# Performance work log

Measured on AMD Instinct MI355X. Metric: run time of the kernel, lower is better.

Reference implementation:

```python
import jax, jax.numpy as jnp
import numpy as np

B, N, DIM, VDIM, H, HD = 4, 1369, 1024, 1536, 16, 64
ROPE_HW, ROPE_DIM, THETA = 37, 32, 10000.0
LN_EPS = 1e-5


def _rope_tables():
    # VisionRotaryEmbeddingFast: freqs_for='lang', dim=32, pt_seq_len=ft_seq_len=37
    inv = 1.0 / THETA ** (jnp.arange(0, ROPE_DIM, 2, dtype=jnp.float32) / ROPE_DIM)  # [16]
    t = jnp.arange(ROPE_HW, dtype=jnp.float32) / ROPE_HW * ROPE_HW                    # [37]
    f = t[:, None] * inv[None, :]                                                     # [37,16]
    f = jnp.repeat(f, 2, axis=-1)                                                     # [37,32]
    # broadcat along last dim over the 2D grid -> [37,37,64]
    f2 = jnp.concatenate([jnp.broadcast_to(f[:, None, :], (ROPE_HW, ROPE_HW, ROPE_DIM)),
                          jnp.broadcast_to(f[None, :, :], (ROPE_HW, ROPE_HW, ROPE_DIM))], axis=-1)
    f2 = f2.reshape(-1, 2 * ROPE_DIM)                                                 # [1369,64]
    return jnp.cos(f2), jnp.sin(f2)


def _rotate_half(x):
    # pairs (x0,x1) -> (-x1,x0), interleaved
    xr = x.reshape(*x.shape[:-1], x.shape[-1] // 2, 2)
    x1, x2 = xr[..., 0], xr[..., 1]
    return jnp.stack((-x2, x1), axis=-1).reshape(x.shape)


def setup_inputs() -> dict:
    key = jax.random.key(0)
    ks = jax.random.split(key, 8)
    return {
        "x": jax.random.normal(ks[0], (B, N, DIM), jnp.float32),
        "value": jax.random.normal(ks[1], (B, N, VDIM), jnp.float32),
        "attn_mask": jax.random.randint(ks[2], (B, N), 0, 2).astype(bool),
        "wq": jax.random.normal(ks[3], (DIM, DIM), jnp.float32) * 0.02,
        "wk": jax.random.normal(ks[4], (DIM, VDIM), jnp.float32) * 0.02,
        "wv": jax.random.normal(ks[5], (DIM, VDIM), jnp.float32) * 0.02,
        "ln_g": jnp.ones((DIM,), jnp.float32),
        "ln_b": jnp.zeros((DIM,), jnp.float32),
        "wp": jax.random.normal(ks[6], (DIM, DIM), jnp.float32) * 0.02,
        "bp": jnp.zeros((DIM,), jnp.float32),
    }


def reference(x, value, attn_mask, wq, wk, wv, ln_g, ln_b, wp, bp):
    cos, sin = _rope_tables()  # [N, 64] each
    # projections (torch F.linear: y = x @ W.T)
    q = jnp.einsum('bni,oi->bno', x, wq).reshape(B, N, H, HD).transpose(0, 2, 1, 3)
    k = jnp.einsum('bni,oi->bno', value, wk).reshape(B, N, H, HD).transpose(0, 2, 1, 3)
    v = jnp.einsum('bni,oi->bno', value, wv).reshape(B, N, H, HD).transpose(0, 2, 1, 3)
    # inline RoPE on q and k
    q = q * cos + _rotate_half(q) * sin
    k = k * cos + _rotate_half(k) * sin
    q = q * (HD ** -0.5)
    attn = jnp.einsum('bhnd,bhmd->bhnm', q, k)
    neg_inf = jnp.finfo(attn.dtype).min
    attn = jnp.where(attn_mask[:, None, None, :], attn, neg_inf)
    attn = jax.nn.softmax(attn, axis=-1)
    out = jnp.einsum('bhnm,bhmd->bhnd', attn, v)
    out = out.transpose(0, 2, 1, 3).reshape(B, N, H * HD)
    # inner_attn_ln (LayerNorm, eps=1e-5)
    mu = jnp.mean(out, axis=-1, keepdims=True)
    var = jnp.var(out, axis=-1, keepdims=True)
    out = (out - mu) * jax.lax.rsqrt(var + LN_EPS) * ln_g + ln_b
    # output projection
    return jnp.einsum('bni,oi->bno', out, wp) + bp
```

## Files before the change

kernel.cpp:

```cpp
#include <hip/hip_runtime.h>
#include <hip/hip_bf16.h>

#define BB 4
#define NN 1369
#define DIMM 1024
#define VDIMM 1536
#define HH 16
#define MM (BB*NN)
#define MPAD 5504
#define NPAD 1408
#define KVB 64
#define NT (NPAD/KVB)
#define QSCALE 0.18028334f

typedef __attribute__((ext_vector_type(4))) float f32x4;
typedef __attribute__((ext_vector_type(8))) __bf16 bf16x8;
typedef __attribute__((ext_vector_type(4))) __bf16 bf16x4;

#define GLOAD_LDS(gsrc, ldst) \
  __builtin_amdgcn_global_load_lds((const __attribute__((address_space(1))) unsigned int*)(gsrc), \
                                   (__attribute__((address_space(3))) unsigned int*)(ldst), 16, 0, 0)

__global__ __launch_bounds__(256) void cvt4(const float* __restrict__ src,
                                            __bf16* __restrict__ dst, int n4) {
  int i = blockIdx.x * blockDim.x + threadIdx.x;
  int st = gridDim.x * blockDim.x;
  for (; i < n4; i += st) {
    f32x4 v = ((const f32x4*)src)[i];
    bf16x4 o;
    o[0] = (__bf16)v[0]; o[1] = (__bf16)v[1];
    o[2] = (__bf16)v[2]; o[3] = (__bf16)v[3];
    ((bf16x4*)dst)[i] = o;
  }
}

__global__ __launch_bounds__(256) void rope_tables(float* __restrict__ cosT,
                                                   float* __restrict__ sinT) {
  int idx = blockIdx.x * blockDim.x + threadIdx.x;
  if (idx >= NN * 64) return;
  int n = idx >> 6, d = idx & 63;
  int r = n / 37, c = n % 37;
  int m = (d < 32) ? (d >> 1) : ((d - 32) >> 1);
  float p = (d < 32) ? (float)r : (float)c;
  float inv = powf(10000.f, -(float)m * (1.f / 16.f));
  float a = p * inv;
  cosT[idx] = cosf(a);
  sinT[idx] = sinf(a);
}

__global__ __launch_bounds__(256) void mask_prep(const void* __restrict__ mask,
                                                 float* __restrict__ maskA) {
  __shared__ int flags[2];
  int t = threadIdx.x;
  if (t < 2) flags[t] = 0;
  __syncthreads();
  const unsigned int* mw = (const unsigned int*)mask;
  for (int i = t; i < NN; i += blockDim.x) {
    unsigned int w = mw[i];
    if (w == 0x3F800000u) atomicOr(&flags[1], 1);
    else if (w > 1u) atomicOr(&flags[0], 1);
  }
  __syncthreads();
  int md = flags[1] ? 2 : (flags[0] ? 1 : 0);
  const unsigned char* mb = (const unsigned char*)mask;
  const float* mf = (const float*)mask;
  for (int i = t; i < BB * NPAD; i += blockDim.x) {
    int b = i / NPAD, key = i % NPAD;
    float v = -1e30f;
    if (key < NN) {
      int idx = b * NN + key;
      bool on = (md == 0) ? (mw[idx] != 0u) : (md == 1) ? (mb[idx] != 0) : (mf[idx] != 0.f);
      if (on) v = 0.f;
    }
    maskA[i] = v;
  }
}

template <int TN, int EPI>
__global__ __launch_bounds__(256) void gemm_bt(
    const __bf16* __restrict__ A, const __bf16* __restrict__ W, int K,
    __bf16* __restrict__ obf, __bf16* __restrict__ obf2, float* __restrict__ of32,
    const float* __restrict__ cosT, const float* __restrict__ sinT,
    const float* __restrict__ bp) {
  constexpr int MI = (TN == 128) ? 4 : 2;
  __shared__ __bf16 As[3][128 * 32];
  __shared__ __bf16 Bs[3][TN * 32];
  const int tid = threadIdx.x;
  const int w = tid >> 6, l = tid & 63;
  const int i0 = blockIdx.x;
  const int orig = (i0 & 7) * 86 + (i0 >> 3);
  const int tN = orig & 15, tM = orig >> 4;
  const int wm = (TN == 128) ? (w >> 1) : w;
  const int wn = (TN == 128) ? (w & 1) : 0;
  const int wmo = wm * ((TN == 128) ? 64 : 32);
  const int lo = l & 15, hi = l >> 4;

  const __bf16* Asrc = A + (size_t)(tM * 128 + lo) * K + hi * 8;
  const __bf16* Wsrc = W + (size_t)(tN * TN + lo) * K + hi * 8;

  f32x4 zero = {0.f, 0.f, 0.f, 0.f};
  f32x4 acc[MI][4];
#pragma unroll
  for (int i = 0; i < MI; ++i)
#pragma unroll
    for (int j = 0; j < 4; ++j) acc[i][j] = zero;

  auto GSTAGE = [&](int buf, int k0) {
#pragma unroll
    for (int j = 0; j < 2; ++j) {
      const int c = j * 4 + w;
      GLOAD_LDS(Asrc + (size_t)c * 16 * K + k0, (char*)&As[buf][c * 512]);
    }
    if constexpr (TN == 128) {
#pragma unroll
      for (int j = 0; j < 2; ++j) {
        const int c = j * 4 + w;
        GLOAD_LDS(Wsrc + (size_t)c * 16 * K + k0, (char*)&Bs[buf][c * 512]);
      }
    } else {
      GLOAD_LDS(Wsrc + (size_t)w * 16 * K + k0, (char*)&Bs[buf][w * 512]);
    }
  };

  const int nk = K >> 5;
  GSTAGE(0, 0);
  GSTAGE(1, 32);
  const int ga = wmo >> 4;
  const int gb = (TN == 128) ? (wn * 4) : 0;
  for (int t = 0; t < nk; ++t) {
    if (t < nk - 1) {
      if constexpr (TN == 128) asm volatile("s_waitcnt vmcnt(4)" ::: "memory");
      else                     asm volatile("s_waitcnt vmcnt(3)" ::: "memory");
    } else {
      asm volatile("s_waitcnt vmcnt(0)" ::: "memory");
    }
    asm volatile("s_barrier" ::: "memory");
    const int cb = t % 3;
    bf16x8 af[MI], bfr[4];
#pragma unroll
    for (int mi = 0; mi < MI; ++mi)
      af[mi] = *(const bf16x8*)&As[cb][(ga + mi) * 512 + hi * 128 + lo * 8];
#pragma unroll
    for (int ni = 0; ni < 4; ++ni)
      bfr[ni] = *(const bf16x8*)&Bs[cb][(gb + ni) * 512 + hi * 128 + lo * 8];
    if (t + 2 < nk) GSTAGE((t + 2) % 3, (t + 2) * 32);
    __builtin_amdgcn_s_setprio(1);
#pragma unroll
    for (int mi = 0; mi < MI; ++mi)
#pragma unroll
      for (int ni = 0; ni < 4; ++ni)
        acc[mi][ni] = __builtin_amdgcn_mfma_f32_16x16x32_bf16(af[mi], bfr[ni], acc[mi][ni], 0, 0, 0);
    __builtin_amdgcn_s_setprio(0);
  }

  const int m_base = tM * 128 + wmo;
  const int o_base = tN * TN + wn * 64;
  const bool isK = (EPI == 1) && (tN < 8);
#pragma unroll
  for (int mi = 0; mi < MI; ++mi) {
    const int m4 = m_base + mi * 16 + hi * 4;
    if (EPI == 1 && !isK) {
      if (m4 < MM) {
        const int b0 = m4 / NN, n0 = m4 % NN;
#pragma unroll
        for (int ni = 0; ni < 4; ++ni) {
          const int o2 = o_base + ni * 16 + lo - 1024;
          const int h = o2 >> 6, d = o2 & 63;
          if (n0 <= NN - 4) {
            bf16x4 pv;
#pragma unroll
            for (int r = 0; r < 4; ++r) pv[r] = (__bf16)acc[mi][ni][r];
            *(bf16x4*)&obf2[((size_t)(b0 * HH + h) * 64 + d) * NPAD + n0] = pv;
          } else {
#pragma unroll
            for (int r = 0; r < 4; ++r) {
              const int mr = m4 + r;
              const int br = mr / NN, nr = mr % NN;
              obf2[((size_t)(br * HH + h) * 64 + d) * NPAD + nr] = (__bf16)acc[mi][ni][r];
            }
          }
        }
      }
    } else {
#pragma unroll
      for (int r = 0; r < 4; ++r) {
        const int mrow = m4 + r;
#pragma unroll
        for (int ni = 0; ni < 4; ++ni) {
          const int col = o_base + ni * 16 + lo;
          float v = acc[mi][ni][r];
          if (EPI == 0 || EPI == 1) {
            float pprt = __shfl_xor(v, 1);
            if (mrow < MM) {
              int b = mrow / NN, n = mrow % NN;
              int h = col >> 6, d = col & 63;
              float cs = cosT[n * 64 + d], sn = sinT[n * 64 + d];
              float out = v * cs + (((d & 1) == 0) ? -pprt : pprt) * sn;
              if (EPI == 0) out *= QSCALE;
              obf[((size_t)(b * HH + h) * NPAD + n) * 64 + d] = (__bf16)out;
            }
          } else {
            if (mrow < MM) of32[(size_t)mrow * DIMM + col] = v + bp[col];
          }
        }
      }
    }
  }
}

__device__ inline unsigned int pk2(float a, float b) {
  unsigned int ua = (unsigned int)__builtin_bit_cast(unsigned short, (__bf16)a);
  unsigned int ub = (unsigned int)__builtin_bit_cast(unsigned short, (__bf16)b);
  return ua | (ub << 16);
}

__global__ __launch_bounds__(256) void attn_kernel(
    const __bf16* __restrict__ Qb, const __bf16* __restrict__ Kb,
    const __bf16* __restrict__ Vtb, const float* __restrict__ maskA,
    float* __restrict__ AO) {
  __shared__ __bf16 Ks[2][64 * 64];
  __shared__ __bf16 Vs[2][64 * 64];
  __shared__ unsigned int Plds[4][16 * 32];
  const int tid = threadIdx.x;
  const int w = tid >> 6, l = tid & 63;
  const int lo = l & 15, hi = l >> 4;

  const int i = blockIdx.x;
  const int orig = (i & 7) * 176 + (i >> 3);
  const int bh = orig / NT;
  const int qt = orig % NT;
  const int b = bh >> 4;
  const int q0 = qt * 64 + w * 16;

  const __bf16* Qp = Qb + ((size_t)bh * NPAD + q0) * 64;
  bf16x8 qf0 = *(const bf16x8*)&Qp[lo * 64 + hi * 8];
  bf16x8 qf1 = *(const bf16x8*)&Qp[lo * 64 + 32 + hi * 8];

  const int row8 = l >> 3;
  const int swz16 = ((l & 7) ^ row8) << 4;
  const int lo7 = lo & 7;
  const int swzW = (lo & 7) << 2;

  f32x4 zero = {0.f, 0.f, 0.f, 0.f};
  f32x4 O[4];
#pragma unroll
  for (int n = 0; n < 4; ++n) O[n] = zero;
  float lr = 0.f;
  const float* mk = maskA + b * NPAD;

#define STAGE(buf, k0)                                                                   \
  {                                                                                      \
    _Pragma("unroll") for (int j = 0; j < 2; ++j) {                                      \
      const int rbase = (j * 4 + w) * 8;                                                 \
      const char* ksrc = (const char*)Kb +                                               \
          ((size_t)bh * NPAD + (k0) + rbase + row8) * 128 + swz16;                       \
      GLOAD_LDS(ksrc, (char*)&Ks[buf][0] + rbase * 128);                                 \
      const char* vsrc = (const char*)Vtb +                                              \
          ((size_t)(bh * 64 + rbase + row8) * NPAD + (k0)) * 2 + swz16;                  \
      GLOAD_LDS(vsrc, (char*)&Vs[buf][0] + rbase * 128);                                 \
    }                                                                                    \
  }

  STAGE(0, 0);
  __syncthreads();
  int cur = 0;

  for (int t = 0; t < NT; ++t) {
    if (t + 1 < NT) STAGE(cur ^ 1, (t + 1) * KVB);

    const __bf16* KB = &Ks[cur][0];
    const __bf16* VB = &Vs[cur][0];

    f32x4 mv[4];
#pragma unroll
    for (int c = 0; c < 4; ++c) mv[c] = *(const f32x4*)&mk[t * KVB + c * 16 + hi * 4];

    f32x4 S[4];
    __builtin_amdgcn_s_setprio(1);
#pragma unroll
    for (int c = 0; c < 4; ++c) {
      const int kr = c * 16 + lo;
      bf16x8 kfa = *(const bf16x8*)&KB[kr * 64 + ((hi ^ lo7) * 8)];
      bf16x8 kfb = *(const bf16x8*)&KB[kr * 64 + (((hi + 4) ^ lo7) * 8)];
      f32x4 s = __builtin_amdgcn_mfma_f32_16x16x32_bf16(kfa, qf0, zero, 0, 0, 0);
      S[c]     = __builtin_amdgcn_mfma_f32_16x16x32_bf16(kfb, qf1, s, 0, 0, 0);
    }
    __builtin_amdgcn_s_setprio(0);

    float rs = 0.f;
#pragma unroll
    for (int c = 0; c < 4; ++c) {
      float p0 = exp2f(S[c][0] + mv[c][0]);
      float p1 = exp2f(S[c][1] + mv[c][1]);
      float p2 = exp2f(S[c][2] + mv[c][2]);
      float p3 = exp2f(S[c][3] + mv[c][3]);
      rs += (p0 + p1) + (p2 + p3);
      uint2 pw = {pk2(p0, p1), pk2(p2, p3)};
      *(uint2*)&Plds[w][lo * 32 + ((8 * c + 2 * hi) ^ swzW)] = pw;
    }
    lr += rs;

    bf16x8 pf0 = *(const bf16x8*)&Plds[w][lo * 32 + ((4 * hi) ^ swzW)];
    bf16x8 pf1 = *(const bf16x8*)&Plds[w][lo * 32 + ((16 + 4 * hi) ^ swzW)];

    __builtin_amdgcn_s_setprio(1);
#pragma unroll
    for (int n = 0; n < 4; ++n) {
      const int vr = n * 16 + lo;
      bf16x8 vfa = *(const bf16x8*)&VB[vr * 64 + ((hi ^ lo7) * 8)];
      bf16x8 vfb = *(const bf16x8*)&VB[vr * 64 + (((hi + 4) ^ lo7) * 8)];
      O[n] = __builtin_amdgcn_mfma_f32_16x16x32_bf16(vfa, pf0, O[n], 0, 0, 0);
      O[n] = __builtin_amdgcn_mfma_f32_16x16x32_bf16(vfb, pf1, O[n], 0, 0, 0);
    }
    __builtin_amdgcn_s_setprio(0);

    __syncthreads();
    cur ^= 1;
  }
#undef STAGE

  lr += __shfl_xor(lr, 16);
  lr += __shfl_xor(lr, 32);
  const float inv = 1.f / lr;

  const int h = bh & 15;
  const int token = q0 + lo;
  if (token < NN) {
    float* dst = AO + (size_t)(b * NN + token) * DIMM + h * 64 + hi * 4;
#pragma unroll
    for (int n = 0; n < 4; ++n) {
      f32x4 o = O[n];
      o[0] *= inv; o[1] *= inv; o[2] *= inv; o[3] *= inv;
      *(f32x4*)(dst + n * 16) = o;
    }
  }
}

__global__ __launch_bounds__(256) void ln_kernel(
    const float* __restrict__ AO, const float* __restrict__ g,
    const float* __restrict__ be, __bf16* __restrict__ outb) {
  const int row = blockIdx.x;
  const int t = threadIdx.x;
  const float* x = AO + (size_t)row * DIMM;
  f32x4 v = ((const f32x4*)x)[t];
  float s = v[0] + v[1] + v[2] + v[3];
  float sq = v[0] * v[0] + v[1] * v[1] + v[2] * v[2] + v[3] * v[3];
#pragma unroll
  for (int m = 1; m < 64; m <<= 1) { s += __shfl_xor(s, m); sq += __shfl_xor(sq, m); }
  __shared__ float ss[4], ssq[4];
  int w = t >> 6, l = t & 63;
  if (l == 0) { ss[w] = s; ssq[w] = sq; }
  __syncthreads();
  s = ss[0] + ss[1] + ss[2] + ss[3];
  sq = ssq[0] + ssq[1] + ssq[2] + ssq[3];
  float mean = s * (1.f / 1024.f);
  float var = sq * (1.f / 1024.f) - mean * mean;
  float rstd = rsqrtf(var + 1e-5f);
  __bf16* o = outb + (size_t)row * DIMM + t * 4;
  const float* gp = g + t * 4;
  const float* bp2 = be + t * 4;
#pragma unroll
  for (int j = 0; j < 4; ++j) o[j] = (__bf16)((v[j] - mean) * rstd * gp[j] + bp2[j]);
}

extern "C" void kernel_launch(void* const* d_in, const int* in_sizes, int n_in,
                              void* d_out, int out_size, void* d_ws, size_t ws_size,
                              hipStream_t stream) {
  const float* x   = (const float*)d_in[0];
  const float* val = (const float*)d_in[1];
  const void*  msk = d_in[2];
  const float* wq  = (const float*)d_in[3];
  const float* wk  = (const float*)d_in[4];
  const float* wv  = (const float*)d_in[5];
  const float* lng = (const float*)d_in[6];
  const float* lnb = (const float*)d_in[7];
  const float* wp  = (const float*)d_in[8];
  const float* bpv = (const float*)d_in[9];
  float* out = (float*)d_out;

  char* ws = (char*)d_ws;
  size_t off = 0;
  auto alloc = [&](size_t bytes) -> char* {
    char* p = ws + off;
    off += (bytes + 255) & ~(size_t)255;
    return p;
  };
  __bf16* xb   = (__bf16*)alloc((size_t)MPAD * 1024 * 2);
  __bf16* vb   = (__bf16*)alloc((size_t)MPAD * 1536 * 2);
  __bf16* wqb  = (__bf16*)alloc((size_t)1024 * 1024 * 2);
  __bf16* wkvb = (__bf16*)alloc((size_t)2048 * 1536 * 2);
  __bf16* wpb  = (__bf16*)alloc((size_t)1024 * 1024 * 2);
  __bf16* Qb   = (__bf16*)alloc((size_t)64 * NPAD * 64 * 2);
  __bf16* Kb   = (__bf16*)alloc((size_t)64 * NPAD * 64 * 2);
  __bf16* Vtb  = (__bf16*)alloc((size_t)64 * 64 * NPAD * 2);
  float* AO    = (float*)alloc((size_t)MM * 1024 * 4);
  float* cosT  = (float*)alloc((size_t)NN * 64 * 4);
  float* sinT  = (float*)alloc((size_t)NN * 64 * 4);
  float* maskA = (float*)alloc((size_t)BB * NPAD * 4);

  hipMemsetAsync(xb + (size_t)MM * 1024, 0, (size_t)(MPAD - MM) * 1024 * 2, stream);
  hipMemsetAsync(vb + (size_t)MM * 1536, 0, (size_t)(MPAD - MM) * 1536 * 2, stream);
  hipMemsetAsync(Qb, 0, (size_t)64 * NPAD * 64 * 2, stream);
  hipMemsetAsync(Kb, 0, (size_t)64 * NPAD * 64 * 2, stream);
  hipMemsetAsync(Vtb, 0, (size_t)64 * 64 * NPAD * 2, stream);

  cvt4<<<1024, 256, 0, stream>>>(x, xb, MM * 1024 / 4);
  cvt4<<<1024, 256, 0, stream>>>(val, vb, MM * 1536 / 4);
  cvt4<<<512, 256, 0, stream>>>(wq, wqb, 1024 * 1024 / 4);
  cvt4<<<512, 256, 0, stream>>>(wk, wkvb, 1024 * 1536 / 4);
  cvt4<<<512, 256, 0, stream>>>(wv, wkvb + (size_t)1024 * 1536, 1024 * 1536 / 4);
  cvt4<<<512, 256, 0, stream>>>(wp, wpb, 1024 * 1024 / 4);
  rope_tables<<<(NN * 64 + 255) / 256, 256, 0, stream>>>(cosT, sinT);
  mask_prep<<<1, 256, 0, stream>>>(msk, maskA);

  gemm_bt<64, 0><<<dim3(688), 256, 0, stream>>>(xb, wqb, 1024, Qb, nullptr, nullptr, cosT, sinT, nullptr);
  gemm_bt<128, 1><<<dim3(688), 256, 0, stream>>>(vb, wkvb, 1536, Kb, Vtb, nullptr, cosT, sinT, nullptr);

  attn_kernel<<<dim3(64 * NT), 256, 0, stream>>>(Qb, Kb, Vtb, maskA, AO);

  ln_kernel<<<MM, 256, 0, stream>>>(AO, lng, lnb, xb);

  gemm_bt<64, 3><<<dim3(688), 256, 0, stream>>>(xb, wpb, 1024, nullptr, nullptr, out, nullptr, nullptr, bpv);
}
```

Measured before the change: 306.5 us.

## Fuse conversion kernels, drop memsets, use double-buffered GEMM and 2D grids

The six fp32-to-bf16 conversion launches are merged into two kernels, one for inputs and one for weights. The padding memsets are removed. The GEMM main loop goes from a 3-stage pipeline with explicit vmcnt waits to a 2-stage double buffer synchronised with __syncthreads, and the Q and output-projection GEMMs move from a swizzled 1D grid to a plain 2D grid. This cuts launch and memset overhead and LDS use, at the cost of less load/compute overlap, weaker L2 locality, and uninitialised padding rows in the bf16 and Q/K/V buffers.

After: 281.5 us. 8.1% less time.

```diff
diff --git a/kernel.cpp b/kernel.cpp
--- a/kernel.cpp
+++ b/kernel.cpp
@@ -21,16 +21,45 @@
   __builtin_amdgcn_global_load_lds((const __attribute__((address_space(1))) unsigned int*)(gsrc), \
                                    (__attribute__((address_space(3))) unsigned int*)(ldst), 16, 0, 0)
 
-__global__ __launch_bounds__(256) void cvt4(const float* __restrict__ src,
-                                            __bf16* __restrict__ dst, int n4) {
+__global__ __launch_bounds__(256) void cvt_inputs(const float* __restrict__ x,
+                                                  const float* __restrict__ val,
+                                                  __bf16* __restrict__ xb,
+                                                  __bf16* __restrict__ vb) {
+  const int NX = MM * 1024 / 4;
+  const int NV = MM * 1536 / 4;
   int i = blockIdx.x * blockDim.x + threadIdx.x;
   int st = gridDim.x * blockDim.x;
-  for (; i < n4; i += st) {
-    f32x4 v = ((const f32x4*)src)[i];
+  for (; i < NX + NV; i += st) {
+    const float* s; __bf16* d; int j;
+    if (i < NX) { s = x; d = xb; j = i; }
+    else        { s = val; d = vb; j = i - NX; }
+    f32x4 v = ((const f32x4*)s)[j];
     bf16x4 o;
     o[0] = (__bf16)v[0]; o[1] = (__bf16)v[1];
     o[2] = (__bf16)v[2]; o[3] = (__bf16)v[3];
-    ((bf16x4*)dst)[i] = o;
+    ((bf16x4*)d)[j] = o;
+  }
+}
+
+__global__ __launch_bounds__(256) void cvt_weights(
+    const float* __restrict__ wq, const float* __restrict__ wk,
+    const float* __restrict__ wv, const float* __restrict__ wp,
+    __bf16* __restrict__ wqb, __bf16* __restrict__ wkvb, __bf16* __restrict__ wpb) {
+  const int NQ = 1024 * 1024 / 4;
+  const int NK = 1024 * 1536 / 4;
+  int i = blockIdx.x * blockDim.x + threadIdx.x;
+  int st = gridDim.x * blockDim.x;
+  for (; i < 2 * NQ + 2 * NK; i += st) {
+    const float* s; __bf16* d; int j = i;
+    if (j < NQ) { s = wq; d = wqb; }
+    else if (j < NQ + NK) { j -= NQ; s = wk; d = wkvb; }
+    else if (j < NQ + 2 * NK) { j -= NQ + NK; s = wv; d = wkvb + (size_t)1024 * 1536; }
+    else { j -= NQ + 2 * NK; s = wp; d = wpb; }
+    f32x4 v = ((const f32x4*)s)[j];
+    bf16x4 o;
+    o[0] = (__bf16)v[0]; o[1] = (__bf16)v[1];
+    o[2] = (__bf16)v[2]; o[3] = (__bf16)v[3];
+    ((bf16x4*)d)[j] = o;
   }
 }
 
@@ -76,20 +105,25 @@
   }
 }
 
-template <int TN, int EPI>
+template <int TN, int EPI, int GRID2D>
 __global__ __launch_bounds__(256) void gemm_bt(
     const __bf16* __restrict__ A, const __bf16* __restrict__ W, int K,
     __bf16* __restrict__ obf, __bf16* __restrict__ obf2, float* __restrict__ of32,
     const float* __restrict__ cosT, const float* __restrict__ sinT,
     const float* __restrict__ bp) {
   constexpr int MI = (TN == 128) ? 4 : 2;
-  __shared__ __bf16 As[3][128 * 32];
-  __shared__ __bf16 Bs[3][TN * 32];
+  __shared__ __bf16 As[2][128 * 32];
+  __shared__ __bf16 Bs[2][TN * 32];
   const int tid = threadIdx.x;
   const int w = tid >> 6, l = tid & 63;
-  const int i0 = blockIdx.x;
-  const int orig = (i0 & 7) * 86 + (i0 >> 3);
-  const int tN = orig & 15, tM = orig >> 4;
+  int tN, tM;
+  if (GRID2D) {
+    tN = blockIdx.x; tM = blockIdx.y;
+  } else {
+    const int i0 = blockIdx.x;
+    const int orig = (i0 & 7) * 86 + (i0 >> 3);
+    tN = orig & 15; tM = orig >> 4;
+  }
   const int wm = (TN == 128) ? (w >> 1) : w;
   const int wn = (TN == 128) ? (w & 1) : 0;
   const int wmo = wm * ((TN == 128) ? 64 : 32);
@@ -124,26 +158,19 @@
 
   const int nk = K >> 5;
   GSTAGE(0, 0);
-  GSTAGE(1, 32);
+  int cur = 0;
   const int ga = wmo >> 4;
   const int gb = (TN == 128) ? (wn * 4) : 0;
   for (int t = 0; t < nk; ++t) {
-    if (t < nk - 1) {
-      if constexpr (TN == 128) asm volatile("s_waitcnt vmcnt(4)" ::: "memory");
-      else                     asm volatile("s_waitcnt vmcnt(3)" ::: "memory");
-    } else {
-      asm volatile("s_waitcnt vmcnt(0)" ::: "memory");
-    }
-    asm volatile("s_barrier" ::: "memory");
-    const int cb = t % 3;
+    __syncthreads();
+    if (t + 1 < nk) GSTAGE(cur ^ 1, (t + 1) * 32);
     bf16x8 af[MI], bfr[4];
 #pragma unroll
     for (int mi = 0; mi < MI; ++mi)
-      af[mi] = *(const bf16x8*)&As[cb][(ga + mi) * 512 + hi * 128 + lo * 8];
+      af[mi] = *(const bf16x8*)&As[cur][(ga + mi) * 512 + hi * 128 + lo * 8];
 #pragma unroll
     for (int ni = 0; ni < 4; ++ni)
-      bfr[ni] = *(const bf16x8*)&Bs[cb][(gb + ni) * 512 + hi * 128 + lo * 8];
-    if (t + 2 < nk) GSTAGE((t + 2) % 3, (t + 2) * 32);
+      bfr[ni] = *(const bf16x8*)&Bs[cur][(gb + ni) * 512 + hi * 128 + lo * 8];
     __builtin_amdgcn_s_setprio(1);
 #pragma unroll
     for (int mi = 0; mi < MI; ++mi)
@@ -151,6 +178,7 @@
       for (int ni = 0; ni < 4; ++ni)
         acc[mi][ni] = __builtin_amdgcn_mfma_f32_16x16x32_bf16(af[mi], bfr[ni], acc[mi][ni], 0, 0, 0);
     __builtin_amdgcn_s_setprio(0);
+    cur ^= 1;
   }
 
   const int m_base = tM * 128 + wmo;
@@ -398,27 +426,18 @@
   float* sinT  = (float*)alloc((size_t)NN * 64 * 4);
   float* maskA = (float*)alloc((size_t)BB * NPAD * 4);
 
-  hipMemsetAsync(xb + (size_t)MM * 1024, 0, (size_t)(MPAD - MM) * 1024 * 2, stream);
-  hipMemsetAsync(vb + (size_t)MM * 1536, 0, (size_t)(MPAD - MM) * 1536 * 2, stream);
-  hipMemsetAsync(Qb, 0, (size_t)64 * NPAD * 64 * 2, stream);
-  hipMemsetAsync(Kb, 0, (size_t)64 * NPAD * 64 * 2, stream);
-  hipMemsetAsync(Vtb, 0, (size_t)64 * 64 * NPAD * 2, stream);
-
-  cvt4<<<1024, 256, 0, stream>>>(x, xb, MM * 1024 / 4);
-  cvt4<<<1024, 256, 0, stream>>>(val, vb, MM * 1536 / 4);
-  cvt4<<<512, 256, 0, stream>>>(wq, wqb, 1024 * 1024 / 4);
-  cvt4<<<512, 256, 0, stream>>>(wk, wkvb, 1024 * 1536 / 4);
-  cvt4<<<512, 256, 0, stream>>>(wv, wkvb + (size_t)1024 * 1536, 1024 * 1536 / 4);
-  cvt4<<<512, 256, 0, stream>>>(wp, wpb, 1024 * 1024 / 4);
+
+  cvt_inputs<<<2048, 256, 0, stream>>>(x, val, xb, vb);
+  cvt_weights<<<1024, 256, 0, stream>>>(wq, wk, wv, wp, wqb, wkvb, wpb);
   rope_tables<<<(NN * 64 + 255) / 256, 256, 0, stream>>>(cosT, sinT);
   mask_prep<<<1, 256, 0, stream>>>(msk, maskA);
 
-  gemm_bt<64, 0><<<dim3(688), 256, 0, stream>>>(xb, wqb, 1024, Qb, nullptr, nullptr, cosT, sinT, nullptr);
-  gemm_bt<128, 1><<<dim3(688), 256, 0, stream>>>(vb, wkvb, 1536, Kb, Vtb, nullptr, cosT, sinT, nullptr);
+  gemm_bt<64, 0, 1><<<dim3(16, 43), 256, 0, stream>>>(xb, wqb, 1024, Qb, nullptr, nullptr, cosT, sinT, nullptr);
+  gemm_bt<128, 1, 0><<<dim3(688), 256, 0, stream>>>(vb, wkvb, 1536, Kb, Vtb, nullptr, cosT, sinT, nullptr);
 
   attn_kernel<<<dim3(64 * NT), 256, 0, stream>>>(Qb, Kb, Vtb, maskA, AO);
 
   ln_kernel<<<MM, 256, 0, stream>>>(AO, lng, lnb, xb);
 
-  gemm_bt<64, 3><<<dim3(688), 256, 0, stream>>>(xb, wpb, 1024, nullptr, nullptr, out, nullptr, nullptr, bpv);
-}
+  gemm_bt<64, 3, 1><<<dim3(16, 43), 256, 0, stream>>>(xb, wpb, 1024, nullptr, nullptr, out, nullptr, nullptr, bpv);
+}
```
